# Kernel optimization log

Hardware: AMD Instinct MI355X
Metric: run time of the kernel (lower is better)

The kernel has to match this reference:

```python
import jax, jax.numpy as jnp
import numpy as np

IN_DIM = 4096
OUT_DIM = 2048
K = 4
R = 4096
B = 4096


def setup_inputs() -> dict:
    key = jax.random.key(0)
    ks = jax.random.split(key, 8)
    s = 0.02
    return {
        "hidden_states": jax.random.normal(ks[0], (B, IN_DIM), jnp.float32),
        # stacked per-block weights, torch Linear layout: W1/W3 [k+1, out, in], W2 [k+1, in, out]
        "W1": jax.random.normal(ks[1], (K + 1, OUT_DIM, IN_DIM), jnp.float32) * s,
        "W3": jax.random.normal(ks[2], (K + 1, OUT_DIM, IN_DIM), jnp.float32) * s,
        "W2": jax.random.normal(ks[3], (K + 1, IN_DIM, OUT_DIM), jnp.float32) * s,
        "fc1_w": jax.random.normal(ks[4], (R, IN_DIM * K), jnp.float32) * s,
        "fc1_b": jax.random.normal(ks[5], (R,), jnp.float32) * s,
        "fc2_w": jax.random.normal(ks[6], (IN_DIM, R), jnp.float32) * s,
        "fc2_b": jax.random.normal(ks[7], (IN_DIM,), jnp.float32) * s,
    }


def reference(hidden_states, W1, W3, W2, fc1_w, fc1_b, fc2_w, fc2_b):
    x = hidden_states
    # batched SwiGLU over k+1 blocks: [B, k+1, out]
    g = jax.nn.silu(jnp.einsum("bi,koi->bko", x, W1)) * jnp.einsum("bi,koi->bko", x, W3)
    wk_outs = jnp.einsum("bko,kio->bki", g, W2)  # [B, k+1, in]
    o0 = wk_outs[:, 0]                            # [B, in]
    concat = wk_outs[:, 1:].reshape(x.shape[0], -1)  # [B, k*in], matches torch.cat order
    h = jax.nn.silu(concat @ fc1_w.T + fc1_b)
    proj = h @ fc2_w.T + fc2_b                    # [B, in]
    diff = o0 - proj
    return (jnp.linalg.norm(diff, ord=2, axis=1), jnp.mean(jnp.abs(diff), axis=1))
```

## Files before the change

kernel.cpp:

```cpp
#include <hip/hip_runtime.h>
#include <hip/hip_bf16.h>
#include <cstdint>
#include <cstddef>

#define IN_DIM 4096
#define OUT_DIM 2048
#define NEXP 5
#define KEXP 4
#define RDIM 4096
#define BATCH 4096

typedef __hip_bfloat16 bf16;
typedef __attribute__((ext_vector_type(8))) short bf16x8;
typedef __attribute__((ext_vector_type(4))) float f32x4;
typedef __attribute__((ext_vector_type(8))) unsigned short u16x8;
typedef __attribute__((ext_vector_type(4))) unsigned short u16x4;

typedef const __attribute__((address_space(1))) unsigned int* as1p;
typedef __attribute__((address_space(3))) unsigned int* as3p;

__device__ __forceinline__ unsigned short f2bf(float x) {
  union { __hip_bfloat16 h; unsigned short u; } cv;
  cv.h = __float2bfloat16(x);
  return cv.u;
}

struct CvtArgs {
  const float* src[6];
  unsigned short* dst[6];
  long long cum[6];
};

__global__ __launch_bounds__(256) void cvt_all_kernel(CvtArgs a, long long tot8) {
  long long c0 = a.cum[0], c1 = a.cum[1], c2 = a.cum[2], c3 = a.cum[3], c4 = a.cum[4];
  for (long long i = (long long)blockIdx.x * 256 + threadIdx.x; i < tot8;
       i += (long long)gridDim.x * 256) {
    int s = (int)(i >= c0) + (i >= c1) + (i >= c2) + (i >= c3) + (i >= c4);
    const float* sp; unsigned short* dp; long long base;
    switch (s) {
      case 0: sp = a.src[0]; dp = a.dst[0]; base = 0;  break;
      case 1: sp = a.src[1]; dp = a.dst[1]; base = c0; break;
      case 2: sp = a.src[2]; dp = a.dst[2]; base = c1; break;
      case 3: sp = a.src[3]; dp = a.dst[3]; base = c2; break;
      case 4: sp = a.src[4]; dp = a.dst[4]; base = c3; break;
      default: sp = a.src[5]; dp = a.dst[5]; base = c4; break;
    }
    long long j = i - base;
    const float4* p = (const float4*)sp;
    float4 va = p[j * 2], vb = p[j * 2 + 1];
    u16x8 v;
    v[0] = f2bf(va.x); v[1] = f2bf(va.y); v[2] = f2bf(va.z); v[3] = f2bf(va.w);
    v[4] = f2bf(vb.x); v[5] = f2bf(vb.y); v[6] = f2bf(vb.z); v[7] = f2bf(vb.w);
    *(u16x8*)(dp + j * 8) = v;
  }
}

__global__ __launch_bounds__(256) void tcvt_kernel(const float* __restrict__ in,
                                                   unsigned short* __restrict__ out,
                                                   int NI, int NO) {
  __shared__ float tile[32][33];
  const float* inz = in + (size_t)blockIdx.z * NI * NO;
  unsigned short* outz = out + (size_t)blockIdx.z * NI * NO;
  int i0 = blockIdx.y * 32;
  int o0 = blockIdx.x * 32;
  int t = threadIdx.x;
  int ri = t >> 3, ro = (t & 7) << 2;
  float4 v = *(const float4*)(inz + (size_t)(i0 + ri) * NO + o0 + ro);
  tile[ri][ro] = v.x; tile[ri][ro + 1] = v.y; tile[ri][ro + 2] = v.z; tile[ri][ro + 3] = v.w;
  __syncthreads();
  int wo = t >> 3, wi = (t & 7) << 2;
  u16x4 w;
  w[0] = f2bf(tile[wi][wo]);
  w[1] = f2bf(tile[wi + 1][wo]);
  w[2] = f2bf(tile[wi + 2][wo]);
  w[3] = f2bf(tile[wi + 3][wo]);
  *(u16x4*)(outz + (size_t)(o0 + wo) * NI + i0 + wi) = w;
}

__device__ __forceinline__ void gload16(const bf16* g, bf16* l) {
  __builtin_amdgcn_global_load_lds((as1p)g, (as3p)l, 16, 0, 0);
}

template <int N> __device__ __forceinline__ void vwait() {
  if constexpr (N == 0) asm volatile("s_waitcnt vmcnt(0)" ::: "memory");
  else if constexpr (N == 2) asm volatile("s_waitcnt vmcnt(2)" ::: "memory");
  else if constexpr (N == 4) asm volatile("s_waitcnt vmcnt(4)" ::: "memory");
}

#define READ_A(buf, mh)                                              \
  do {                                                               \
    const bf16* _pa = ldsA + (buf) * 16384 + (mh) * 8192;            \
    _Pragma("unroll") for (int m2 = 0; m2 < 4; ++m2) {               \
      afr[m2][0] = *(const bf16x8*)(_pa + aOff[m2]);                 \
      afr[m2][1] = *(const bf16x8*)(_pa + (aOff[m2] ^ 32));          \
    }                                                                \
  } while (0)

#define READ_B(buf, nh)                                              \
  do {                                                               \
    const bf16* _pb = ldsB + (buf) * 16384 + (nh) * 8192;            \
    _Pragma("unroll") for (int n2 = 0; n2 < 2; ++n2) {               \
      bfr[(nh) * 2 + n2][0] = *(const bf16x8*)(_pb + bOff[(nh) * 2 + n2]);        \
      bfr[(nh) * 2 + n2][1] = *(const bf16x8*)(_pb + (bOff[(nh) * 2 + n2] ^ 32)); \
    }                                                                \
  } while (0)

#define QMFMA(mh, nh)                                                            \
  do {                                                                           \
    __builtin_amdgcn_s_setprio(1);                                               \
    _Pragma("unroll") for (int m2 = 0; m2 < 4; ++m2) {                           \
      _Pragma("unroll") for (int n2 = 0; n2 < 2; ++n2) {                         \
        acc[(mh) * 4 + m2][(nh) * 2 + n2] = __builtin_amdgcn_mfma_f32_16x16x32_bf16( \
            afr[m2][0], bfr[(nh) * 2 + n2][0], acc[(mh) * 4 + m2][(nh) * 2 + n2], 0, 0, 0); \
        acc[(mh) * 4 + m2][(nh) * 2 + n2] = __builtin_amdgcn_mfma_f32_16x16x32_bf16( \
            afr[m2][1], bfr[(nh) * 2 + n2][1], acc[(mh) * 4 + m2][(nh) * 2 + n2], 0, 0, 0); \
      }                                                                          \
    }                                                                            \
    __builtin_amdgcn_s_setprio(0);                                               \
  } while (0)

#define BAR() __builtin_amdgcn_s_barrier()

template <int EPI>
__global__ __launch_bounds__(512, 2) void gemm8p(
    const bf16* __restrict__ A, int lda, long long aZ,
    const bf16* __restrict__ B, int ldb, long long bZ,
    int Kdim,
    const bf16* __restrict__ A2, int lda2,
    const bf16* __restrict__ B2, int ldb2,
    int Kdim2,
    unsigned short* __restrict__ C, int ldc, long long cZ,
    const float* __restrict__ bias,
    float* __restrict__ accum,
    int gx, int gxy, int nwg8) {
  extern __shared__ __align__(16) bf16 lds[];
  bf16* ldsA = lds;
  bf16* ldsB = lds + 32768;

  int flat = blockIdx.x;
  int wg = (flat & 7) * nwg8 + (flat >> 3);
  int z = wg / gxy;
  int r0 = wg - z * gxy;
  int by = r0 / gx;
  int bx = r0 - by * gx;
  int rowBase = by * 256, colBase = bx * 256;

  int tid = threadIdx.x;
  int wave = tid >> 6, lane = tid & 63;
  int wr = wave >> 2, wc = wave & 3;

  int rl = tid >> 3;
  int cg8 = ((tid & 7) ^ (rl & 7)) << 3;
  int dstOfs = wave * 512;

  int aOff[4], bOff[4];
#pragma unroll
  for (int m2 = 0; m2 < 4; ++m2) {
    int rA = ((2 * m2 + wr) * 16) + (lane & 15);
    aOff[m2] = rA * 64 + (((lane >> 4) ^ (rA & 7)) << 3);
  }
#pragma unroll
  for (int n = 0; n < 4; ++n) {
    int rB = (((4 * n + wc) * 16) & 127) + (lane & 15);
    bOff[n] = rB * 64 + (((lane >> 4) ^ (rB & 7)) << 3);
  }

  f32x4 acc[8][4] = {};
  bf16x8 afr[4][2], bfr[4][2];

  auto runK = [&](const bf16* AbT, int lda_, const bf16* BbT, int ldb_, int NT) {
    int srcA = rl * lda_ + cg8;
    int srcB = rl * ldb_ + cg8;
    auto stA = [&](int buf, int hh, int kt) {
      const bf16* s = AbT + (long long)(hh * 128) * lda_ + kt * 64;
      bf16* d = ldsA + buf * 16384 + hh * 8192 + dstOfs;
      gload16(s + srcA, d);
      gload16(s + srcA + 64 * lda_, d + 4096);
    };
    auto stB = [&](int buf, int hh, int kt) {
      const bf16* s = BbT + (long long)(hh * 128) * ldb_ + kt * 64;
      bf16* d = ldsB + buf * 16384 + hh * 8192 + dstOfs;
      gload16(s + srcB, d);
      gload16(s + srcB + 64 * ldb_, d + 4096);
    };

    int cur = 0;
    stA(0, 0, 0); stB(0, 0, 0); stB(0, 1, 0); stA(0, 1, 0);
    vwait<4>();
    BAR();

    for (int t = 0; t < NT - 1; ++t) {
      int nb = cur ^ 1;
      READ_A(cur, 0);
      READ_B(cur, 0);
      stA(nb, 0, t + 1);
      vwait<4>();
      BAR();
      QMFMA(0, 0);
      READ_B(cur, 1);
      stB(nb, 0, t + 1);
      vwait<4>();
      BAR();
      QMFMA(0, 1);
      READ_A(cur, 1);
      stB(nb, 1, t + 1);
      BAR();
      QMFMA(1, 1);
      stA(nb, 1, t + 1);
      vwait<4>();
      BAR();
      QMFMA(1, 0);
      cur = nb;
    }

    READ_A(cur, 0);
    READ_B(cur, 0);
    vwait<2>();
    BAR();
    QMFMA(0, 0);
    READ_B(cur, 1);
    vwait<0>();
    BAR();
    QMFMA(0, 1);
    READ_A(cur, 1);
    QMFMA(1, 1);
    QMFMA(1, 0);
    BAR();
  };

  runK(A + (long long)z * aZ + (long long)rowBase * lda, lda,
       B + (long long)z * bZ + (long long)colBase * ldb, ldb,
       Kdim >> 6);
  if constexpr (EPI == 2) {
    runK(A2 + (long long)rowBase * lda2, lda2,
         B2 + (long long)colBase * ldb2, ldb2,
         Kdim2 >> 6);
  }

  if constexpr (EPI == 2) {
#pragma unroll
    for (int m = 0; m < 8; ++m) {
#pragma unroll
      for (int r = 0; r < 4; ++r) {
        int row = rowBase + (2 * m + wr) * 16 + ((lane >> 4) << 2) + r;
        float ssq = 0.f, sab = 0.f;
#pragma unroll
        for (int n = 0; n < 4; ++n) {
          int col = colBase + (4 * n + wc) * 16 + (lane & 15);
          float d = acc[m][n][r] - bias[col];
          ssq += d * d;
          sab += fabsf(d);
        }
#pragma unroll
        for (int off = 1; off < 16; off <<= 1) {
          ssq += __shfl_xor(ssq, off);
          sab += __shfl_xor(sab, off);
        }
        if ((lane & 15) == 0) {
          atomicAdd(&accum[row], ssq);
          atomicAdd(&accum[BATCH + row], sab);
        }
      }
    }
  } else {
    unsigned short* Cb = C + (long long)z * cZ;
#pragma unroll
    for (int m = 0; m < 8; ++m) {
#pragma unroll
      for (int n = 0; n < 4; ++n) {
        int col = colBase + (4 * n + wc) * 16 + (lane & 15);
#pragma unroll
        for (int r = 0; r < 4; ++r) {
          int row = rowBase + (2 * m + wr) * 16 + ((lane >> 4) << 2) + r;
          float v = acc[m][n][r];
          if constexpr (EPI == 1) {
            v += bias[col];
            v = -(v / (1.f + __expf(-v)));
          }
          Cb[(long long)row * ldc + col] = f2bf(v);
        }
      }
    }
  }
}

#define READ_B1(buf)                                                  \
  do {                                                                \
    const bf16* _pb = ldsB1 + (buf) * 8192;                           \
    _Pragma("unroll") for (int n2 = 0; n2 < 2; ++n2) {                \
      b1fr[n2][0] = *(const bf16x8*)(_pb + bOff[n2]);                 \
      b1fr[n2][1] = *(const bf16x8*)(_pb + (bOff[n2] ^ 32));          \
    }                                                                 \
  } while (0)

#define READ_B3(buf)                                                  \
  do {                                                                \
    const bf16* _pb = ldsB3 + (buf) * 8192;                           \
    _Pragma("unroll") for (int n2 = 0; n2 < 2; ++n2) {                \
      b3fr[n2][0] = *(const bf16x8*)(_pb + bOff[n2]);                 \
      b3fr[n2][1] = *(const bf16x8*)(_pb + (bOff[n2] ^ 32));          \
    }                                                                 \
  } while (0)

#define QMFMA_D(ACC, mh, BF)                                                     \
  do {                                                                           \
    __builtin_amdgcn_s_setprio(1);                                               \
    _Pragma("unroll") for (int m2 = 0; m2 < 4; ++m2) {                           \
      _Pragma("unroll") for (int n2 = 0; n2 < 2; ++n2) {                         \
        ACC[(mh) * 4 + m2][n2] = __builtin_amdgcn_mfma_f32_16x16x32_bf16(        \
            afr[m2][0], BF[n2][0], ACC[(mh) * 4 + m2][n2], 0, 0, 0);             \
        ACC[(mh) * 4 + m2][n2] = __builtin_amdgcn_mfma_f32_16x16x32_bf16(        \
            afr[m2][1], BF[n2][1], ACC[(mh) * 4 + m2][n2], 0, 0, 0);             \
      }                                                                          \
    }                                                                            \
    __builtin_amdgcn_s_setprio(0);                                               \
  } while (0)

__global__ __launch_bounds__(512, 2) void gemm_dual(
    const bf16* __restrict__ A,
    const bf16* __restrict__ W1b, const bf16* __restrict__ W3b,
    unsigned short* __restrict__ G,
    int gx, int gxy, int nwg8) {
  extern __shared__ __align__(16) bf16 lds[];
  bf16* ldsA = lds;
  bf16* ldsB1 = lds + 32768;
  bf16* ldsB3 = lds + 49152;

  int flat = blockIdx.x;
  int wg = (flat & 7) * nwg8 + (flat >> 3);
  int z = wg / gxy;
  int r0 = wg - z * gxy;
  int by = r0 / gx;
  int bx = r0 - by * gx;
  int rowBase = by * 256, colBase = bx * 128;

  int tid = threadIdx.x;
  int wave = tid >> 6, lane = tid & 63;
  int wr = wave >> 2, wc = wave & 3;

  const bf16* Ab = A + (long long)rowBase * IN_DIM;
  const bf16* B1b = W1b + (long long)z * OUT_DIM * IN_DIM + (long long)colBase * IN_DIM;
  const bf16* B3b = W3b + (long long)z * OUT_DIM * IN_DIM + (long long)colBase * IN_DIM;

  int rl = tid >> 3;
  int cg8 = ((tid & 7) ^ (rl & 7)) << 3;
  int src = rl * IN_DIM + cg8;
  int dstOfs = wave * 512;

  int aOff[4], bOff[2];
#pragma unroll
  for (int m2 = 0; m2 < 4; ++m2) {
    int rA = ((2 * m2 + wr) * 16) + (lane & 15);
    aOff[m2] = rA * 64 + (((lane >> 4) ^ (rA & 7)) << 3);
  }
#pragma unroll
  for (int n2 = 0; n2 < 2; ++n2) {
    int rB = (4 * n2 + wc) * 16 + (lane & 15);
    bOff[n2] = rB * 64 + (((lane >> 4) ^ (rB & 7)) << 3);
  }

  f32x4 acc1[8][2] = {};
  f32x4 acc2[8][2] = {};
  bf16x8 afr[4][2], b1fr[2][2], b3fr[2][2];

  auto stA = [&](int buf, int hh, int kt) {
    const bf16* s = Ab + (long long)(hh * 128) * IN_DIM + kt * 64;
    bf16* d = ldsA + buf * 16384 + hh * 8192 + dstOfs;
    gload16(s + src, d);
    gload16(s + src + 64 * IN_DIM, d + 4096);
  };
  auto stB1 = [&](int buf, int kt) {
    const bf16* s = B1b + kt * 64;
    bf16* d = ldsB1 + buf * 8192 + dstOfs;
    gload16(s + src, d);
    gload16(s + src + 64 * IN_DIM, d + 4096);
  };
  auto stB3 = [&](int buf, int kt) {
    const bf16* s = B3b + kt * 64;
    bf16* d = ldsB3 + buf * 8192 + dstOfs;
    gload16(s + src, d);
    gload16(s + src + 64 * IN_DIM, d + 4096);
  };

  const int NT = IN_DIM >> 6;
  int cur = 0;

  stA(0, 0, 0); stB1(0, 0); stB3(0, 0); stA(0, 1, 0);
  vwait<4>();
  BAR();

  for (int t = 0; t < NT - 1; ++t) {
    int nb = cur ^ 1;
    READ_A(cur, 0);
    READ_B1(cur);
    stA(nb, 0, t + 1);
    vwait<4>();
    BAR();
    QMFMA_D(acc1, 0, b1fr);
    READ_B3(cur);
    stB1(nb, t + 1);
    vwait<4>();
    BAR();
    QMFMA_D(acc2, 0, b3fr);
    READ_A(cur, 1);
    stB3(nb, t + 1);
    BAR();
    QMFMA_D(acc1, 1, b1fr);
    stA(nb, 1, t + 1);
    vwait<4>();
    BAR();
    QMFMA_D(acc2, 1, b3fr);
    cur = nb;
  }

  READ_A(cur, 0);
  READ_B1(cur);
  vwait<2>();
  BAR();
  QMFMA_D(acc1, 0, b1fr);
  READ_B3(cur);
  vwait<0>();
  BAR();
  QMFMA_D(acc2, 0, b3fr);
  READ_A(cur, 1);
  QMFMA_D(acc1, 1, b1fr);
  QMFMA_D(acc2, 1, b3fr);

  unsigned short* Gb = G + (long long)z * OUT_DIM;
#pragma unroll
  for (int m = 0; m < 8; ++m) {
#pragma unroll
    for (int n2 = 0; n2 < 2; ++n2) {
      int col = colBase + (4 * n2 + wc) * 16 + (lane & 15);
#pragma unroll
      for (int r = 0; r < 4; ++r) {
        int row = rowBase + (2 * m + wr) * 16 + ((lane >> 4) << 2) + r;
        float v1 = acc1[m][n2][r], v2 = acc2[m][n2][r];
        float g = v2 * (v1 / (1.f + __expf(-v1)));
        Gb[(long long)row * (NEXP * OUT_DIM) + col] = f2bf(g);
      }
    }
  }
}

__global__ void zero_accum(float* a) {
  int i = blockIdx.x * 256 + threadIdx.x;
  if (i < 2 * BATCH) a[i] = 0.f;
}

__global__ void finalize_kernel(const float* __restrict__ accum, float* __restrict__ out) {
  int b = blockIdx.x * 256 + threadIdx.x;
  if (b < BATCH) {
    out[b] = sqrtf(accum[b]);
    out[BATCH + b] = accum[BATCH + b] * (1.f / IN_DIM);
  }
}

extern "C" void kernel_launch(void* const* d_in, const int* in_sizes, int n_in,
                              void* d_out, int out_size, void* d_ws, size_t ws_size,
                              hipStream_t stream) {
  const float* x    = (const float*)d_in[0];
  const float* W1   = (const float*)d_in[1];
  const float* W3   = (const float*)d_in[2];
  const float* W2   = (const float*)d_in[3];
  const float* fc1w = (const float*)d_in[4];
  const float* fc1b = (const float*)d_in[5];
  const float* fc2w = (const float*)d_in[6];
  const float* fc2b = (const float*)d_in[7];
  float* out = (float*)d_out;

  char* ws = (char*)d_ws;
  size_t off = 0;
  auto alloc = [&](size_t bytes) {
    char* p = ws + off;
    off += (bytes + 255) & ~(size_t)255;
    return p;
  };
  bf16* xb   = (bf16*)alloc((size_t)BATCH * IN_DIM * 2);
  bf16* w1b  = (bf16*)alloc((size_t)NEXP * OUT_DIM * IN_DIM * 2);
  bf16* w3b  = (bf16*)alloc((size_t)NEXP * OUT_DIM * IN_DIM * 2);
  bf16* w2b0 = (bf16*)alloc((size_t)IN_DIM * OUT_DIM * 2);
  bf16* w2t  = (bf16*)alloc((size_t)KEXP * OUT_DIM * IN_DIM * 2);
  bf16* f1b  = (bf16*)alloc((size_t)RDIM * IN_DIM * KEXP * 2);
  bf16* f2b  = (bf16*)alloc((size_t)IN_DIM * RDIM * 2);
  bf16* gbuf = (bf16*)alloc((size_t)BATCH * NEXP * OUT_DIM * 2);
  bf16* Pcat = (bf16*)alloc((size_t)RDIM * KEXP * OUT_DIM * 2);
  bf16* hbuf = (bf16*)alloc((size_t)BATCH * RDIM * 2);
  float* accum = (float*)alloc((size_t)2 * BATCH * 4);
  if (off > ws_size) return;

  {
    CvtArgs a;
    long long n8[6] = {
        (long long)BATCH * IN_DIM / 8,
        (long long)NEXP * OUT_DIM * IN_DIM / 8,
        (long long)NEXP * OUT_DIM * IN_DIM / 8,
        (long long)IN_DIM * OUT_DIM / 8,
        (long long)RDIM * IN_DIM * KEXP / 8,
        (long long)IN_DIM * RDIM / 8};
    const float* srcs[6] = {x, W1, W3, W2, fc1w, fc2w};
    unsigned short* dsts[6] = {(unsigned short*)xb, (unsigned short*)w1b,
                               (unsigned short*)w3b, (unsigned short*)w2b0,
                               (unsigned short*)f1b, (unsigned short*)f2b};
    long long c = 0;
    for (int i = 0; i < 6; ++i) {
      a.src[i] = srcs[i]; a.dst[i] = dsts[i];
      c += n8[i]; a.cum[i] = c;
    }
    cvt_all_kernel<<<2048, 256, 0, stream>>>(a, c);
  }
  tcvt_kernel<<<dim3(OUT_DIM / 32, IN_DIM / 32, KEXP), 256, 0, stream>>>(
      W2 + (size_t)IN_DIM * OUT_DIM, (unsigned short*)w2t, IN_DIM, OUT_DIM);
  zero_accum<<<(2 * BATCH + 255) / 256, 256, 0, stream>>>(accum);

  const size_t LDSB = 131072;

  {
    int gx = OUT_DIM / 128, gxy = gx * (BATCH / 256), nwg = gxy * NEXP;
    gemm_dual<<<nwg, 512, LDSB, stream>>>(
        xb, w1b, w3b, (unsigned short*)gbuf, gx, gxy, nwg / 8);
  }
  {
    int gx = OUT_DIM / 256, gxy = gx * (RDIM / 256), nwg = gxy * KEXP;
    gemm8p<0><<<nwg, 512, LDSB, stream>>>(
        f1b, KEXP * IN_DIM, (long long)IN_DIM,
        w2t, IN_DIM, (long long)OUT_DIM * IN_DIM,
        IN_DIM,
        nullptr, 0, nullptr, 0, 0,
        (unsigned short*)Pcat, KEXP * OUT_DIM, (long long)OUT_DIM,
        nullptr, nullptr,
        gx, gxy, nwg / 8);
  }
  {
    int gx = RDIM / 256, gxy = gx * (BATCH / 256), nwg = gxy;
    gemm8p<1><<<nwg, 512, LDSB, stream>>>(
        gbuf + OUT_DIM, NEXP * OUT_DIM, 0LL,
        Pcat, KEXP * OUT_DIM, 0LL,
        KEXP * OUT_DIM,
        nullptr, 0, nullptr, 0, 0,
        (unsigned short*)hbuf, RDIM, 0LL,
        fc1b, nullptr,
        gx, gxy, nwg / 8);
  }
  {
    int gx = IN_DIM / 256, gxy = gx * (BATCH / 256), nwg = gxy;
    gemm8p<2><<<nwg, 512, LDSB, stream>>>(
        gbuf, NEXP * OUT_DIM, 0LL,
        w2b0, OUT_DIM, 0LL,
        OUT_DIM,
        hbuf, RDIM,
        f2b, RDIM,
        RDIM,
        nullptr, 0, 0LL,
        fc2b, accum,
        gx, gxy, nwg / 8);
  }
  finalize_kernel<<<(BATCH + 255) / 256, 256, 0, stream>>>(accum, out);
}
```

Measured before the change: 1.392 ms.

## Restructure GEMM main loops into deeper prefetch pipeline with explicit LDS waits

Both GEMM main loops (generic and fused SwiGLU) now unroll over pairs of K-tiles with fixed buffer indices. Global-to-LDS loads for the next tile are issued earlier, and vmcnt is relaxed to 6 outstanding loads, so more memory traffic is in flight while MFMAs run. Each LDS fragment read is followed by an explicit lgkmcnt(0) wait plus a sched_barrier, and barriers bracket every MFMA quarter, which is a ping-pong style schedule. This deepens overlap of loads with compute at the cost of many more barriers and rigid scheduling. It also assumes NT is even.

```diff
diff --git a/kernel.cpp b/kernel.cpp
--- a/kernel.cpp
+++ b/kernel.cpp
@@ -83,8 +83,12 @@
 
 template <int N> __device__ __forceinline__ void vwait() {
   if constexpr (N == 0) asm volatile("s_waitcnt vmcnt(0)" ::: "memory");
-  else if constexpr (N == 2) asm volatile("s_waitcnt vmcnt(2)" ::: "memory");
-  else if constexpr (N == 4) asm volatile("s_waitcnt vmcnt(4)" ::: "memory");
+  else if constexpr (N == 6) asm volatile("s_waitcnt vmcnt(6)" ::: "memory");
+}
+
+__device__ __forceinline__ void lgkm0() {
+  asm volatile("s_waitcnt lgkmcnt(0)" ::: "memory");
+  __builtin_amdgcn_sched_barrier(0);
 }
 
 #define READ_A(buf, mh)                                              \
@@ -184,46 +188,55 @@
       gload16(s + srcB + 64 * ldb_, d + 4096);
     };
 
-    int cur = 0;
+    int NP = NT >> 1;
     stA(0, 0, 0); stB(0, 0, 0); stB(0, 1, 0); stA(0, 1, 0);
-    vwait<4>();
+    stA(1, 0, 1); stB(1, 0, 1); stB(1, 1, 1);
+    vwait<6>();
     BAR();
 
-    for (int t = 0; t < NT - 1; ++t) {
-      int nb = cur ^ 1;
-      READ_A(cur, 0);
-      READ_B(cur, 0);
-      stA(nb, 0, t + 1);
-      vwait<4>();
-      BAR();
-      QMFMA(0, 0);
-      READ_B(cur, 1);
-      stB(nb, 0, t + 1);
-      vwait<4>();
-      BAR();
-      QMFMA(0, 1);
-      READ_A(cur, 1);
-      stB(nb, 1, t + 1);
-      BAR();
-      QMFMA(1, 1);
-      stA(nb, 1, t + 1);
-      vwait<4>();
-      BAR();
-      QMFMA(1, 0);
-      cur = nb;
+    for (int i = 0; i < NP - 1; ++i) {
+      int t = 2 * i;
+      READ_A(0, 0); READ_B(0, 0);
+      stA(1, 1, t + 1);
+      BAR(); lgkm0(); QMFMA(0, 0); BAR();
+      READ_B(0, 1);
+      stA(0, 0, t + 2);
+      BAR(); lgkm0(); QMFMA(0, 1); BAR();
+      READ_A(0, 1);
+      stB(0, 0, t + 2);
+      BAR(); lgkm0(); QMFMA(1, 1); BAR();
+      stB(0, 1, t + 2);
+      vwait<6>();
+      BAR(); QMFMA(1, 0); BAR();
+      READ_A(1, 0); READ_B(1, 0);
+      stA(0, 1, t + 2);
+      BAR(); lgkm0(); QMFMA(0, 0); BAR();
+      READ_B(1, 1);
+      stA(1, 0, t + 3);
+      BAR(); lgkm0(); QMFMA(0, 1); BAR();
+      READ_A(1, 1);
+      stB(1, 0, t + 3);
+      BAR(); lgkm0(); QMFMA(1, 1); BAR();
+      stB(1, 1, t + 3);
+      vwait<6>();
+      BAR(); QMFMA(1, 0); BAR();
     }
 
-    READ_A(cur, 0);
-    READ_B(cur, 0);
-    vwait<2>();
-    BAR();
-    QMFMA(0, 0);
-    READ_B(cur, 1);
+    READ_A(0, 0); READ_B(0, 0);
+    stA(1, 1, NT - 1);
+    BAR(); lgkm0(); QMFMA(0, 0); BAR();
+    READ_B(0, 1);
+    BAR(); lgkm0(); QMFMA(0, 1); BAR();
+    READ_A(0, 1);
+    BAR(); lgkm0(); QMFMA(1, 1); BAR();
     vwait<0>();
-    BAR();
-    QMFMA(0, 1);
-    READ_A(cur, 1);
-    QMFMA(1, 1);
+    BAR(); QMFMA(1, 0); BAR();
+    READ_A(1, 0); READ_B(1, 0);
+    BAR(); lgkm0(); QMFMA(0, 0); BAR();
+    READ_B(1, 1);
+    BAR(); lgkm0(); QMFMA(0, 1); BAR();
+    READ_A(1, 1);
+    BAR(); lgkm0(); QMFMA(1, 1); BAR();
     QMFMA(1, 0);
     BAR();
   };
@@ -383,47 +396,56 @@
   };
 
   const int NT = IN_DIM >> 6;
-  int cur = 0;
+  const int NP = NT >> 1;
 
   stA(0, 0, 0); stB1(0, 0); stB3(0, 0); stA(0, 1, 0);
-  vwait<4>();
+  stA(1, 0, 1); stB1(1, 1); stB3(1, 1);
+  vwait<6>();
   BAR();
 
-  for (int t = 0; t < NT - 1; ++t) {
-    int nb = cur ^ 1;
-    READ_A(cur, 0);
-    READ_B1(cur);
-    stA(nb, 0, t + 1);
-    vwait<4>();
-    BAR();
-    QMFMA_D(acc1, 0, b1fr);
-    READ_B3(cur);
-    stB1(nb, t + 1);
-    vwait<4>();
-    BAR();
-    QMFMA_D(acc2, 0, b3fr);
-    READ_A(cur, 1);
-    stB3(nb, t + 1);
-    BAR();
-    QMFMA_D(acc1, 1, b1fr);
-    stA(nb, 1, t + 1);
-    vwait<4>();
-    BAR();
-    QMFMA_D(acc2, 1, b3fr);
-    cur = nb;
-  }
-
-  READ_A(cur, 0);
-  READ_B1(cur);
-  vwait<2>();
-  BAR();
-  QMFMA_D(acc1, 0, b1fr);
-  READ_B3(cur);
+  for (int i = 0; i < NP - 1; ++i) {
+    int t = 2 * i;
+    READ_A(0, 0); READ_B1(0);
+    stA(1, 1, t + 1);
+    BAR(); lgkm0(); QMFMA_D(acc1, 0, b1fr); BAR();
+    READ_B3(0);
+    stA(0, 0, t + 2);
+    BAR(); lgkm0(); QMFMA_D(acc2, 0, b3fr); BAR();
+    READ_A(0, 1);
+    stB1(0, t + 2);
+    BAR(); lgkm0(); QMFMA_D(acc1, 1, b1fr); BAR();
+    stB3(0, t + 2);
+    vwait<6>();
+    BAR(); QMFMA_D(acc2, 1, b3fr); BAR();
+    READ_A(1, 0); READ_B1(1);
+    stA(0, 1, t + 2);
+    BAR(); lgkm0(); QMFMA_D(acc1, 0, b1fr); BAR();
+    READ_B3(1);
+    stA(1, 0, t + 3);
+    BAR(); lgkm0(); QMFMA_D(acc2, 0, b3fr); BAR();
+    READ_A(1, 1);
+    stB1(1, t + 3);
+    BAR(); lgkm0(); QMFMA_D(acc1, 1, b1fr); BAR();
+    stB3(1, t + 3);
+    vwait<6>();
+    BAR(); QMFMA_D(acc2, 1, b3fr); BAR();
+  }
+
+  READ_A(0, 0); READ_B1(0);
+  stA(1, 1, NT - 1);
+  BAR(); lgkm0(); QMFMA_D(acc1, 0, b1fr); BAR();
+  READ_B3(0);
+  BAR(); lgkm0(); QMFMA_D(acc2, 0, b3fr); BAR();
+  READ_A(0, 1);
+  BAR(); lgkm0(); QMFMA_D(acc1, 1, b1fr); BAR();
   vwait<0>();
-  BAR();
-  QMFMA_D(acc2, 0, b3fr);
-  READ_A(cur, 1);
-  QMFMA_D(acc1, 1, b1fr);
+  BAR(); QMFMA_D(acc2, 1, b3fr); BAR();
+  READ_A(1, 0); READ_B1(1);
+  BAR(); lgkm0(); QMFMA_D(acc1, 0, b1fr); BAR();
+  READ_B3(1);
+  BAR(); lgkm0(); QMFMA_D(acc2, 0, b3fr); BAR();
+  READ_A(1, 1);
+  BAR(); lgkm0(); QMFMA_D(acc1, 1, b1fr); BAR();
   QMFMA_D(acc2, 1, b3fr);
 
   unsigned short* Gb = G + (long long)z * OUT_DIM;
```

Measured after the change: 1.433 ms. 1.03x slower.

## Fuse fp32-to-bf16 conversion of W1/W3/fc1_w into GEMM operand loads

Applied to the files above, without the earlier changes.

Drops the separate bf16 conversion pass for W1, W3 and fc1_w. gemm_dual and a new gemm_a32 kernel now read fp32 directly into registers, convert, and write bf16 into LDS, replacing async global-to-LDS loads for those operands. This removes a large conversion write and re-read of roughly 210M elements. In exchange, each GEMM tile reads twice the bytes, since fp32 weights are reread by every row-block, and the pipeline uses register staging with extra LDS waits plus a relaxed occupancy launch bound.

```diff
diff --git a/kernel.cpp b/kernel.cpp
--- a/kernel.cpp
+++ b/kernel.cpp
@@ -25,33 +25,33 @@
   return cv.u;
 }
 
+__device__ __forceinline__ u16x8 pack8(float4 a, float4 b) {
+  u16x8 v;
+  v[0] = f2bf(a.x); v[1] = f2bf(a.y); v[2] = f2bf(a.z); v[3] = f2bf(a.w);
+  v[4] = f2bf(b.x); v[5] = f2bf(b.y); v[6] = f2bf(b.z); v[7] = f2bf(b.w);
+  return v;
+}
+
 struct CvtArgs {
-  const float* src[6];
-  unsigned short* dst[6];
-  long long cum[6];
+  const float* src[3];
+  unsigned short* dst[3];
+  long long cum[3];
 };
 
 __global__ __launch_bounds__(256) void cvt_all_kernel(CvtArgs a, long long tot8) {
-  long long c0 = a.cum[0], c1 = a.cum[1], c2 = a.cum[2], c3 = a.cum[3], c4 = a.cum[4];
+  long long c0 = a.cum[0], c1 = a.cum[1];
   for (long long i = (long long)blockIdx.x * 256 + threadIdx.x; i < tot8;
        i += (long long)gridDim.x * 256) {
-    int s = (int)(i >= c0) + (i >= c1) + (i >= c2) + (i >= c3) + (i >= c4);
+    int s = (int)(i >= c0) + (i >= c1);
     const float* sp; unsigned short* dp; long long base;
     switch (s) {
       case 0: sp = a.src[0]; dp = a.dst[0]; base = 0;  break;
       case 1: sp = a.src[1]; dp = a.dst[1]; base = c0; break;
-      case 2: sp = a.src[2]; dp = a.dst[2]; base = c1; break;
-      case 3: sp = a.src[3]; dp = a.dst[3]; base = c2; break;
-      case 4: sp = a.src[4]; dp = a.dst[4]; base = c3; break;
-      default: sp = a.src[5]; dp = a.dst[5]; base = c4; break;
+      default: sp = a.src[2]; dp = a.dst[2]; base = c1; break;
     }
     long long j = i - base;
     const float4* p = (const float4*)sp;
-    float4 va = p[j * 2], vb = p[j * 2 + 1];
-    u16x8 v;
-    v[0] = f2bf(va.x); v[1] = f2bf(va.y); v[2] = f2bf(va.z); v[3] = f2bf(va.w);
-    v[4] = f2bf(vb.x); v[5] = f2bf(vb.y); v[6] = f2bf(vb.z); v[7] = f2bf(vb.w);
-    *(u16x8*)(dp + j * 8) = v;
+    *(u16x8*)(dp + j * 8) = pack8(p[j * 2], p[j * 2 + 1]);
   }
 }
 
@@ -85,6 +85,10 @@
   if constexpr (N == 0) asm volatile("s_waitcnt vmcnt(0)" ::: "memory");
   else if constexpr (N == 2) asm volatile("s_waitcnt vmcnt(2)" ::: "memory");
   else if constexpr (N == 4) asm volatile("s_waitcnt vmcnt(4)" ::: "memory");
+}
+
+__device__ __forceinline__ void lgkm0() {
+  asm volatile("s_waitcnt lgkmcnt(0)" ::: "memory");
 }
 
 #define READ_A(buf, mh)                                              \
@@ -284,6 +288,136 @@
   }
 }
 
+__global__ __launch_bounds__(512) void gemm_a32(
+    const float* __restrict__ A, int lda, long long aZ,
+    const bf16* __restrict__ B, int ldb, long long bZ,
+    int Kdim,
+    unsigned short* __restrict__ C, int ldc, long long cZ,
+    int gx, int gxy, int nwg8) {
+  extern __shared__ __align__(16) bf16 lds[];
+  bf16* ldsA = lds;
+  bf16* ldsB = lds + 32768;
+
+  int flat = blockIdx.x;
+  int wg = (flat & 7) * nwg8 + (flat >> 3);
+  int z = wg / gxy;
+  int r0 = wg - z * gxy;
+  int by = r0 / gx;
+  int bx = r0 - by * gx;
+  int rowBase = by * 256, colBase = bx * 256;
+
+  int tid = threadIdx.x;
+  int wave = tid >> 6, lane = tid & 63;
+  int wr = wave >> 2, wc = wave & 3;
+
+  const float* Af = A + (long long)z * aZ + (long long)rowBase * lda;
+  const bf16* Bb = B + (long long)z * bZ + (long long)colBase * ldb;
+
+  int rl = tid >> 3;
+  int cg8 = ((tid & 7) ^ (rl & 7)) << 3;
+  int srcA32 = rl * lda + cg8;
+  int srcB = rl * ldb + cg8;
+  int dstOfs = wave * 512;
+
+  int aOff[4], bOff[4];
+#pragma unroll
+  for (int m2 = 0; m2 < 4; ++m2) {
+    int rA = ((2 * m2 + wr) * 16) + (lane & 15);
+    aOff[m2] = rA * 64 + (((lane >> 4) ^ (rA & 7)) << 3);
+  }
+#pragma unroll
+  for (int n = 0; n < 4; ++n) {
+    int rB = (((4 * n + wc) * 16) & 127) + (lane & 15);
+    bOff[n] = rB * 64 + (((lane >> 4) ^ (rB & 7)) << 3);
+  }
+
+  f32x4 acc[8][4] = {};
+  bf16x8 afr[4][2], bfr[4][2];
+  float4 rLo[4], rHi[4];
+
+  auto ldA32 = [&](float4* r, int hh, int kt) {
+    const float* s = Af + (long long)(hh * 128) * lda + kt * 64 + srcA32;
+    r[0] = *(const float4*)(s);
+    r[1] = *(const float4*)(s + 4);
+    r[2] = *(const float4*)(s + (long long)64 * lda);
+    r[3] = *(const float4*)(s + (long long)64 * lda + 4);
+  };
+  auto wrA = [&](int buf, int hh, const float4* r) {
+    bf16* d = ldsA + buf * 16384 + hh * 8192;
+    *(u16x8*)(d + tid * 8) = pack8(r[0], r[1]);
+    *(u16x8*)(d + 4096 + tid * 8) = pack8(r[2], r[3]);
+  };
+  auto stB = [&](int buf, int hh, int kt) {
+    const bf16* s = Bb + (long long)(hh * 128) * ldb + kt * 64;
+    bf16* d = ldsB + buf * 16384 + hh * 8192 + dstOfs;
+    gload16(s + srcB, d);
+    gload16(s + srcB + 64 * ldb, d + 4096);
+  };
+
+  int NT = Kdim >> 6;
+  int cur = 0;
+
+  ldA32(rLo, 0, 0);
+  stB(0, 0, 0); stB(0, 1, 0);
+  wrA(0, 0, rLo);
+  ldA32(rHi, 1, 0);
+  lgkm0();
+  BAR();
+
+  for (int t = 0; t < NT - 1; ++t) {
+    int nb = cur ^ 1;
+    wrA(cur, 1, rHi);
+    READ_A(cur, 0);
+    READ_B(cur, 0);
+    lgkm0();
+    BAR();
+    QMFMA(0, 0);
+    READ_B(cur, 1);
+    stB(nb, 0, t + 1);
+    BAR();
+    QMFMA(0, 1);
+    READ_A(cur, 1);
+    stB(nb, 1, t + 1);
+    ldA32(rLo, 0, t + 1);
+    BAR();
+    QMFMA(1, 1);
+    wrA(nb, 0, rLo);
+    ldA32(rHi, 1, t + 1);
+    lgkm0();
+    BAR();
+    QMFMA(1, 0);
+    cur = nb;
+  }
+
+  wrA(cur, 1, rHi);
+  READ_A(cur, 0);
+  READ_B(cur, 0);
+  lgkm0();
+  BAR();
+  QMFMA(0, 0);
+  READ_B(cur, 1);
+  BAR();
+  QMFMA(0, 1);
+  READ_A(cur, 1);
+  BAR();
+  QMFMA(1, 1);
+  QMFMA(1, 0);
+
+  unsigned short* Cb = C + (long long)z * cZ;
+#pragma unroll
+  for (int m = 0; m < 8; ++m) {
+#pragma unroll
+    for (int n = 0; n < 4; ++n) {
+      int col = colBase + (4 * n + wc) * 16 + (lane & 15);
+#pragma unroll
+      for (int r = 0; r < 4; ++r) {
+        int row = rowBase + (2 * m + wr) * 16 + ((lane >> 4) << 2) + r;
+        Cb[(long long)row * ldc + col] = f2bf(acc[m][n][r]);
+      }
+    }
+  }
+}
+
 #define READ_B1(buf)                                                  \
   do {                                                                \
     const bf16* _pb = ldsB1 + (buf) * 8192;                           \
@@ -316,9 +450,9 @@
     __builtin_amdgcn_s_setprio(0);                                               \
   } while (0)
 
-__global__ __launch_bounds__(512, 2) void gemm_dual(
+__global__ __launch_bounds__(512) void gemm_dual(
     const bf16* __restrict__ A,
-    const bf16* __restrict__ W1b, const bf16* __restrict__ W3b,
+    const float* __restrict__ W1f, const float* __restrict__ W3f,
     unsigned short* __restrict__ G,
     int gx, int gxy, int nwg8) {
   extern __shared__ __align__(16) bf16 lds[];
@@ -339,8 +473,8 @@
   int wr = wave >> 2, wc = wave & 3;
 
   const bf16* Ab = A + (long long)rowBase * IN_DIM;
-  const bf16* B1b = W1b + (long long)z * OUT_DIM * IN_DIM + (long long)colBase * IN_DIM;
-  const bf16* B3b = W3b + (long long)z * OUT_DIM * IN_DIM + (long long)colBase * IN_DIM;
+  const float* B1f = W1f + (long long)z * OUT_DIM * IN_DIM + (long long)colBase * IN_DIM;
+  const float* B3f = W3f + (long long)z * OUT_DIM * IN_DIM + (long long)colBase * IN_DIM;
 
   int rl = tid >> 3;
   int cg8 = ((tid & 7) ^ (rl & 7)) << 3;
@@ -362,6 +496,7 @@
   f32x4 acc1[8][2] = {};
   f32x4 acc2[8][2] = {};
   bf16x8 afr[4][2], b1fr[2][2], b3fr[2][2];
+  float4 r1[4], r3[4];
 
   auto stA = [&](int buf, int hh, int kt) {
     const bf16* s = Ab + (long long)(hh * 128) * IN_DIM + kt * 64;
@@ -369,24 +504,28 @@
     gload16(s + src, d);
     gload16(s + src + 64 * IN_DIM, d + 4096);
   };
-  auto stB1 = [&](int buf, int kt) {
-    const bf16* s = B1b + kt * 64;
-    bf16* d = ldsB1 + buf * 8192 + dstOfs;
-    gload16(s + src, d);
-    gload16(s + src + 64 * IN_DIM, d + 4096);
-  };
-  auto stB3 = [&](int buf, int kt) {
-    const bf16* s = B3b + kt * 64;
-    bf16* d = ldsB3 + buf * 8192 + dstOfs;
-    gload16(s + src, d);
-    gload16(s + src + 64 * IN_DIM, d + 4096);
+  auto ldB = [&](float4* r, const float* Bf, int kt) {
+    const float* s = Bf + kt * 64 + src;
+    r[0] = *(const float4*)(s);
+    r[1] = *(const float4*)(s + 4);
+    r[2] = *(const float4*)(s + (long long)64 * IN_DIM);
+    r[3] = *(const float4*)(s + (long long)64 * IN_DIM + 4);
+  };
+  auto wrB = [&](bf16* base, int buf, const float4* r) {
+    bf16* d = base + buf * 8192;
+    *(u16x8*)(d + tid * 8) = pack8(r[0], r[1]);
+    *(u16x8*)(d + 4096 + tid * 8) = pack8(r[2], r[3]);
   };
 
   const int NT = IN_DIM >> 6;
   int cur = 0;
 
-  stA(0, 0, 0); stB1(0, 0); stB3(0, 0); stA(0, 1, 0);
-  vwait<4>();
+  stA(0, 0, 0); stA(0, 1, 0);
+  ldB(r1, B1f, 0);
+  ldB(r3, B3f, 0);
+  wrB(ldsB1, 0, r1);
+  wrB(ldsB3, 0, r3);
+  lgkm0();
   BAR();
 
   for (int t = 0; t < NT - 1; ++t) {
@@ -394,35 +533,36 @@
     READ_A(cur, 0);
     READ_B1(cur);
     stA(nb, 0, t + 1);
-    vwait<4>();
+    ldB(r1, B1f, t + 1);
     BAR();
     QMFMA_D(acc1, 0, b1fr);
+    wrB(ldsB1, nb, r1);
     READ_B3(cur);
-    stB1(nb, t + 1);
-    vwait<4>();
+    ldB(r3, B3f, t + 1);
+    lgkm0();
     BAR();
     QMFMA_D(acc2, 0, b3fr);
+    wrB(ldsB3, nb, r3);
     READ_A(cur, 1);
-    stB3(nb, t + 1);
+    lgkm0();
     BAR();
     QMFMA_D(acc1, 1, b1fr);
     stA(nb, 1, t + 1);
-    vwait<4>();
     BAR();
     QMFMA_D(acc2, 1, b3fr);
     cur = nb;
   }
 
+  vwait<0>();
   READ_A(cur, 0);
   READ_B1(cur);
-  vwait<2>();
   BAR();
   QMFMA_D(acc1, 0, b1fr);
   READ_B3(cur);
-  vwait<0>();
   BAR();
   QMFMA_D(acc2, 0, b3fr);
   READ_A(cur, 1);
+  BAR();
   QMFMA_D(acc1, 1, b1fr);
   QMFMA_D(acc2, 1, b3fr);
 
@@ -477,11 +617,8 @@
     return p;
   };
   bf16* xb   = (bf16*)alloc((size_t)BATCH * IN_DIM * 2);
-  bf16* w1b  = (bf16*)alloc((size_t)NEXP * OUT_DIM * IN_DIM * 2);
-  bf16* w3b  = (bf16*)alloc((size_t)NEXP * OUT_DIM * IN_DIM * 2);
   bf16* w2b0 = (bf16*)alloc((size_t)IN_DIM * OUT_DIM * 2);
   bf16* w2t  = (bf16*)alloc((size_t)KEXP * OUT_DIM * IN_DIM * 2);
-  bf16* f1b  = (bf16*)alloc((size_t)RDIM * IN_DIM * KEXP * 2);
   bf16* f2b  = (bf16*)alloc((size_t)IN_DIM * RDIM * 2);
   bf16* gbuf = (bf16*)alloc((size_t)BATCH * NEXP * OUT_DIM * 2);
   bf16* Pcat = (bf16*)alloc((size_t)RDIM * KEXP * OUT_DIM * 2);
@@ -491,19 +628,15 @@
 
   {
     CvtArgs a;
-    long long n8[6] = {
+    long long n8[3] = {
         (long long)BATCH * IN_DIM / 8,
-        (long long)NEXP * OUT_DIM * IN_DIM / 8,
-        (long long)NEXP * OUT_DIM * IN_DIM / 8,
         (long long)IN_DIM * OUT_DIM / 8,
-        (long long)RDIM * IN_DIM * KEXP / 8,
         (long long)IN_DIM * RDIM / 8};
-    const float* srcs[6] = {x, W1, W3, W2, fc1w, fc2w};
-    unsigned short* dsts[6] = {(unsigned short*)xb, (unsigned short*)w1b,
-                               (unsigned short*)w3b, (unsigned short*)w2b0,
-                               (unsigned short*)f1b, (unsigned short*)f2b};
+    const float* srcs[3] = {x, W2, fc2w};
+    unsigned short* dsts[3] = {(unsigned short*)xb, (unsigned short*)w2b0,
+                               (unsigned short*)f2b};
     long long c = 0;
-    for (int i = 0; i < 6; ++i) {
+    for (int i = 0; i < 3; ++i) {
       a.src[i] = srcs[i]; a.dst[i] = dsts[i];
       c += n8[i]; a.cum[i] = c;
     }
@@ -518,17 +651,15 @@
   {
     int gx = OUT_DIM / 128, gxy = gx * (BATCH / 256), nwg = gxy * NEXP;
     gemm_dual<<<nwg, 512, LDSB, stream>>>(
-        xb, w1b, w3b, (unsigned short*)gbuf, gx, gxy, nwg / 8);
+        xb, W1, W3, (unsigned short*)gbuf, gx, gxy, nwg / 8);
   }
   {
     int gx = OUT_DIM / 256, gxy = gx * (RDIM / 256), nwg = gxy * KEXP;
-    gemm8p<0><<<nwg, 512, LDSB, stream>>>(
-        f1b, KEXP * IN_DIM, (long long)IN_DIM,
+    gemm_a32<<<nwg, 512, LDSB, stream>>>(
+        fc1w, KEXP * IN_DIM, (long long)IN_DIM,
         w2t, IN_DIM, (long long)OUT_DIM * IN_DIM,
         IN_DIM,
-        nullptr, 0, nullptr, 0, 0,
         (unsigned short*)Pcat, KEXP * OUT_DIM, (long long)OUT_DIM,
-        nullptr, nullptr,
         gx, gxy, nwg / 8);
   }
   {
```

Measured after the change: 1.731 ms. +24.4%, slower.
